# Kernel tuning notes

Measured on AMD Instinct MI355X. Metric: run time of the kernel, lower is better.

Reference implementation:

```python
import jax, jax.numpy as jnp
import numpy as np

# Architecture constants (match init_kwargs)
A = 4            # num_areas
E_PER = 512      # excitatory units per area
I_PER = 128      # inhibitory units per area
H = A * (E_PER + I_PER)   # 2560 hidden units, order: [all E (area-major), all I]
NUM_OBJS = 2
IN_UNITS = 64
IN = NUM_OBJS * IN_UNITS  # 128 input units
DT, TAU_X = 0.02, 0.1
ALPHA_X = DT / TAU_X


def _build_masks():
    """Signed Dale's-law connectivity masks, as in _get_connectivity_mask_* ."""
    # inter-area recurrent connectivity: nearest-neighbor hierarchy + self
    rec = np.eye(A) + np.eye(A, k=1) + np.eye(A, k=-1)
    ee = np.kron(rec, np.ones((E_PER, E_PER)))
    ei = np.kron(np.eye(A), np.ones((E_PER, I_PER)))   # E<-I only within area
    ie = np.kron(rec, np.ones((I_PER, E_PER)))
    ii = np.kron(np.eye(A), np.ones((I_PER, I_PER)))
    conn = np.block([[ee, ei], [ie, ii]])
    # sign mask: first e_size columns excitatory (+1), rest inhibitory (-1)
    sign = np.concatenate([np.ones(A * E_PER), -np.ones(A * I_PER)])[None, :]
    rec_mask = conn * sign
    np.fill_diagonal(rec_mask, 0.0)  # remove_diag=True in h2h EILinear
    # input mask: only area 0 receives external input; e_prop=1 for x2h (all +1)
    in_area = np.zeros((A, NUM_OBJS)); in_area[0, :] = 1.0
    in_e = np.kron(in_area, np.ones((E_PER, IN_UNITS)))
    in_i = np.kron(in_area, np.ones((I_PER, IN_UNITS)))
    in_mask = np.concatenate([in_e, in_i], axis=0)
    return jnp.asarray(rec_mask, jnp.float32), jnp.asarray(in_mask, jnp.float32)


def setup_inputs() -> dict:
    key = jax.random.key(0)
    k1, k2, k3 = jax.random.split(key, 3)
    T, B = 500, 64
    inputs = jax.random.normal(k1, (T, B, IN), dtype=jnp.float32)
    W_rec = jax.random.normal(k2, (H, H), dtype=jnp.float32) / np.sqrt(H)
    b_rec = jnp.zeros((H,), dtype=jnp.float32)
    W_in = jax.random.normal(k3, (H, IN), dtype=jnp.float32) / np.sqrt(IN)
    return {"inputs": inputs, "W_rec": W_rec, "b_rec": b_rec, "W_in": W_in}


def reference(inputs, W_rec, b_rec, W_in):
    rec_mask, in_mask = _build_masks()
    # EILinear effective weights: pos_func=abs, times signed connectivity mask
    W_rec_eff = jnp.abs(W_rec) * rec_mask          # [H, H]
    W_in_eff = jnp.abs(W_in) * in_mask             # [H, IN]
    # input projection for all timesteps at once
    proj = jnp.einsum('tbi,hi->tbh', inputs, W_in_eff)  # [T, B, H]

    def retanh(x):
        return jnp.tanh(jax.nn.relu(x))

    def step(carry, u_t):
        x, r = carry
        pre = r @ W_rec_eff.T + b_rec + u_t        # h2h(r) + x2h(u)
        x = (1.0 - ALPHA_X) * x + ALPHA_X * pre    # leaky integration
        r = retanh(x)
        return (x, r), r

    B = inputs.shape[1]
    x0 = jnp.zeros((B, H), dtype=inputs.dtype)     # x0 (train_init_state=False)
    (_, _), rates = jax.lax.scan(step, (x0, retanh(x0)), proj)
    return rates  # [T, B, H] firing rates
```

## Files before the change

kernel.cpp:

```cpp
#include <hip/hip_runtime.h>
#include <math.h>

#define Hn   2560
#define Bn   64
#define INW  128
#define ETOT 2048
#define HGn  160
#define MAXC 13
#define NBLK 160
#define MAXI 7
#define RFSTRIDE (80 * 4 * 512)

typedef __attribute__((ext_vector_type(8))) _Float16 half8;
typedef __attribute__((ext_vector_type(4))) float  floatx4;

__global__ void build_apack(const float* __restrict__ Wrec,
                            const float* __restrict__ Win,
                            _Float16* __restrict__ Af) {
  int hg = blockIdx.x, c = blockIdx.y;
  int a = (hg < 128) ? (hg >> 5) : ((hg - 128) >> 3);
  int nE = (a == 0 || a == 3) ? 8 : 12;
  int nch = nE + 1 + (a == 0 ? 1 : 0);
  if (c >= nch) return;
  int h0 = hg * 16;
  int tid = threadIdx.x;
  int kq = tid >> 6, L = tid & 63;
  int m = L & 15, q = L >> 4;
  int h = h0 + m;

  const float* src; int k0, stride; float sgn; bool isIn = false;
  if (c < nE)       { k0 = ((a == 0 ? 0 : a - 1) << 9) + (c << 7); src = Wrec; stride = Hn;  sgn =  1.f; }
  else if (c == nE) { k0 = ETOT + (a << 7);                        src = Wrec; stride = Hn;  sgn = -1.f; }
  else              { k0 = 0;                                      src = Win;  stride = INW; sgn =  1.f; isIn = true; }

  _Float16 hi8[8], lo8[8];
  #pragma unroll
  for (int j = 0; j < 8; ++j) {
    int k = k0 + kq * 32 + q * 8 + j;
    float w = fabsf(src[(size_t)h * stride + k]);
    if (!isIn && k == h) w = 0.f;
    w *= sgn;
    _Float16 wh = (_Float16)w;
    hi8[j] = wh;
    lo8[j] = (_Float16)(w - (float)wh);
  }
  _Float16* outp = Af + (size_t)(hg * MAXC + c) * 4096;
  *(uint4*)(outp + (kq * 2 + 0) * 512 + L * 8) = *(const uint4*)hi8;
  *(uint4*)(outp + (kq * 2 + 1) * 512 + L * 8) = *(const uint4*)lo8;
}

#define LOAD4(B0,B1,B2,B3,P) \
  asm volatile("global_load_dwordx4 %0, %4, off sc0 sc1\n\t" \
               "global_load_dwordx4 %1, %4, off offset:1024 sc0 sc1\n\t" \
               "global_load_dwordx4 %2, %4, off offset:2048 sc0 sc1\n\t" \
               "global_load_dwordx4 %3, %4, off offset:3072 sc0 sc1\n\t" \
               "s_waitcnt vmcnt(0)" \
               : "=&v"(B0), "=&v"(B1), "=&v"(B2), "=&v"(B3) \
               : "v"(P) : "memory")

#define LOAD8(X0,X1,X2,X3,Y0,Y1,Y2,Y3,PA,PB) \
  asm volatile("global_load_dwordx4 %0, %8, off sc0 sc1\n\t" \
               "global_load_dwordx4 %1, %8, off offset:1024 sc0 sc1\n\t" \
               "global_load_dwordx4 %2, %8, off offset:2048 sc0 sc1\n\t" \
               "global_load_dwordx4 %3, %8, off offset:3072 sc0 sc1\n\t" \
               "global_load_dwordx4 %4, %9, off sc0 sc1\n\t" \
               "global_load_dwordx4 %5, %9, off offset:1024 sc0 sc1\n\t" \
               "global_load_dwordx4 %6, %9, off offset:2048 sc0 sc1\n\t" \
               "global_load_dwordx4 %7, %9, off offset:3072 sc0 sc1\n\t" \
               "s_waitcnt vmcnt(0)" \
               : "=&v"(X0), "=&v"(X1), "=&v"(X2), "=&v"(X3), \
                 "=&v"(Y0), "=&v"(Y1), "=&v"(Y2), "=&v"(Y3) \
               : "v"(PA), "v"(PB) : "memory")

#define MFMA8(i, B0,B1,B2,B3) do { \
  ac0 = __builtin_amdgcn_mfma_f32_16x16x32_f16(ah[i], B0, ac0, 0, 0, 0); \
  ac0 = __builtin_amdgcn_mfma_f32_16x16x32_f16(al[i], B0, ac0, 0, 0, 0); \
  ac1 = __builtin_amdgcn_mfma_f32_16x16x32_f16(ah[i], B1, ac1, 0, 0, 0); \
  ac1 = __builtin_amdgcn_mfma_f32_16x16x32_f16(al[i], B1, ac1, 0, 0, 0); \
  ac2 = __builtin_amdgcn_mfma_f32_16x16x32_f16(ah[i], B2, ac2, 0, 0, 0); \
  ac2 = __builtin_amdgcn_mfma_f32_16x16x32_f16(al[i], B2, ac2, 0, 0, 0); \
  ac3 = __builtin_amdgcn_mfma_f32_16x16x32_f16(ah[i], B3, ac3, 0, 0, 0); \
  ac3 = __builtin_amdgcn_mfma_f32_16x16x32_f16(al[i], B3, ac3, 0, 0, 0); \
} while (0)

#define RECPATH1(i) do { \
  half8 B0_, B1_, B2_, B3_; \
  const _Float16* pp_ = rs + boff[i]; \
  LOAD4(B0_, B1_, B2_, B3_, pp_); \
  MFMA8(i, B0_, B1_, B2_, B3_); \
} while (0)

#define INPATH(i) do { \
  const float* ip_ = inputs + (size_t)t * (Bn * INW) + boff[i]; \
  int nb_ = L & 15; \
  half8 B0_, B1_, B2_, B3_; \
  _Pragma("unroll") for (int j = 0; j < 8; ++j) B0_[j] = (_Float16)ip_[(nb_ +  0) * INW + j]; \
  _Pragma("unroll") for (int j = 0; j < 8; ++j) B1_[j] = (_Float16)ip_[(nb_ + 16) * INW + j]; \
  _Pragma("unroll") for (int j = 0; j < 8; ++j) B2_[j] = (_Float16)ip_[(nb_ + 32) * INW + j]; \
  _Pragma("unroll") for (int j = 0; j < 8; ++j) B3_[j] = (_Float16)ip_[(nb_ + 48) * INW + j]; \
  MFMA8(i, B0_, B1_, B2_, B3_); \
} while (0)

#define PAIR(i0, i1) do { \
  bool r0_ = act[i0] && !isin[i0]; \
  bool r1_ = act[i1] && !isin[i1]; \
  if (r0_ && r1_) { \
    half8 X0_,X1_,X2_,X3_,Y0_,Y1_,Y2_,Y3_; \
    const _Float16* pa_ = rs + boff[i0]; \
    const _Float16* pb_ = rs + boff[i1]; \
    LOAD8(X0_,X1_,X2_,X3_,Y0_,Y1_,Y2_,Y3_, pa_, pb_); \
    MFMA8(i0, X0_, X1_, X2_, X3_); \
    MFMA8(i1, Y0_, Y1_, Y2_, Y3_); \
  } else { \
    if (r0_) RECPATH1(i0); else if (act[i0]) INPATH(i0); \
    if (r1_) RECPATH1(i1); else if (act[i1]) INPATH(i1); \
  } \
} while (0)

template <int ROT>
__global__ __launch_bounds__(512, ROT ? 1 : 2) void rnn_persist(
    const _Float16* __restrict__ Af,
    const float* __restrict__ inputs,
    _Float16* __restrict__ rfbase,
    const float* __restrict__ brec,
    float* __restrict__ rates,
    unsigned* bar, int T)
{
  __shared__ float red[8][1056];
  __shared__ float rrt[16][68];
  __shared__ float bb[16];

  const int bid = blockIdx.x;
  int hg_;
  if (ROT) {
    int x = bid & 7, aa = x >> 1, idx = (x & 1) * 20 + (bid >> 3);
    hg_ = (idx < 32) ? (aa * 32 + idx) : (128 + aa * 8 + (idx - 32));
  } else {
    hg_ = bid;
  }
  const int hg  = hg_;
  const int tid = threadIdx.x;
  const int w   = tid >> 6, L = tid & 63;
  const int h0  = hg * 16;
  const int a   = (hg < 128) ? (hg >> 5) : ((hg - 128) >> 3);
  const int nE  = (a == 0 || a == 3) ? 8 : 12;
  const int SK  = (nE + 1 + (a == 0 ? 1 : 0)) * 4;
  const int ktE0 = (a == 0 ? 0 : a - 1) * 16;
  const int ktI0 = 64 + a * 4;

  unsigned* bsub = bar + (hg & 7) * 64;
  unsigned* bmas = bar + 8 * 64;
  unsigned* bgen = bar + (9 + (hg & 7)) * 64;

  if (tid < 16) bb[tid] = brec[h0 + tid];

  half8 ah[MAXI], al[MAXI];
  int   boff[MAXI];
  bool  act[MAXI], isin[MAXI];
  const _Float16* Abase = Af + (size_t)hg * MAXC * 4096;
  #pragma unroll
  for (int i = 0; i < MAXI; ++i) {
    half8 zz = {0,0,0,0,0,0,0,0};
    ah[i] = zz; al[i] = zz;
    int ks = w + i * 8;
    act[i]  = ks < SK;
    isin[i] = false;
    boff[i] = 0;
    if (act[i]) {
      int c = ks >> 2, kq = ks & 3;
      const _Float16* Ap = Abase + (size_t)c * 4096 + (size_t)(kq * 2) * 512 + (size_t)L * 8;
      ah[i] = *(const half8*)Ap;
      al[i] = *(const half8*)(Ap + 512);
      if (c <= nE) {
        int kt = (c < nE) ? (ktE0 + c * 4 + kq) : (ktI0 + kq);
        boff[i] = kt * 2048 + L * 8;
      } else {
        isin[i] = true;
        boff[i] = kq * 32 + (L >> 4) * 8;
      }
    }
  }
  #pragma unroll
  for (int i = 0; i < MAXI; ++i)
    asm volatile("" : "+v"(ah[i]), "+v"(al[i]));

  float xv[2] = {0.f, 0.f};

  __syncthreads();

  for (int t = 0; t < T; ++t) {
    const _Float16* __restrict__ rs;
    _Float16* __restrict__ rd;
    if (ROT) {
      rs = rfbase + (size_t)t * RFSTRIDE;
      rd = rfbase + (size_t)(t + 1) * RFSTRIDE;
    } else {
      rs = (t & 1) ? (rfbase + RFSTRIDE) : rfbase;
      rd = (t & 1) ? rfbase : (rfbase + RFSTRIDE);
    }

    floatx4 ac0 = {0.f,0.f,0.f,0.f}, ac1 = {0.f,0.f,0.f,0.f};
    floatx4 ac2 = {0.f,0.f,0.f,0.f}, ac3 = {0.f,0.f,0.f,0.f};

    if (ROT) {
      #pragma unroll
      for (int i = 0; i < MAXI; ++i) {
        if (!act[i]) continue;
        half8 b0, b1, b2, b3;
        if (isin[i]) {
          const float* ip = inputs + (size_t)t * (Bn * INW) + boff[i];
          int nb = L & 15;
          #pragma unroll
          for (int j = 0; j < 8; ++j) b0[j] = (_Float16)ip[(nb +  0) * INW + j];
          #pragma unroll
          for (int j = 0; j < 8; ++j) b1[j] = (_Float16)ip[(nb + 16) * INW + j];
          #pragma unroll
          for (int j = 0; j < 8; ++j) b2[j] = (_Float16)ip[(nb + 32) * INW + j];
          #pragma unroll
          for (int j = 0; j < 8; ++j) b3[j] = (_Float16)ip[(nb + 48) * INW + j];
        } else {
          const _Float16* Bp = rs + boff[i];
          b0 = *(const half8*)(Bp);
          b1 = *(const half8*)(Bp + 512);
          b2 = *(const half8*)(Bp + 1024);
          b3 = *(const half8*)(Bp + 1536);
        }
        MFMA8(i, b0, b1, b2, b3);
      }
    } else {
      PAIR(0, 1);
      PAIR(2, 3);
      PAIR(4, 5);
      if (act[6]) { if (!isin[6]) RECPATH1(6); else INPATH(6); }
    }

    #pragma unroll
    for (int p = 0; p < 4; ++p) {
      int m = (L >> 4) * 4 + p;
      float* rw = &red[w][m * 66 + (L & 15)];
      rw[ 0] = ac0[p];
      rw[16] = ac1[p];
      rw[32] = ac2[p];
      rw[48] = ac3[p];
    }
    __syncthreads();

    #pragma unroll
    for (int e = 0; e < 2; ++e) {
      int elem = tid + e * 512;
      int m = elem >> 6, n = elem & 63;
      float s = 0.f;
      #pragma unroll
      for (int j = 0; j < 8; ++j) s += red[j][m * 66 + n];
      float x = 0.8f * xv[e] + 0.2f * (s + bb[m]);
      xv[e] = x;
      float xr = fmaxf(x, 0.f);
      float e2 = __builtin_amdgcn_exp2f(xr * 2.885390081777926814f);
      rrt[m][n] = 1.0f - 2.0f * __builtin_amdgcn_rcpf(e2 + 1.0f);
    }
    __syncthreads();

    if (tid < 128) {
      int bt = tid >> 5, Lq = tid & 31;
      int Lp = (hg & 1) * 32 + Lq;
      half8 vv;
      #pragma unroll
      for (int j = 0; j < 8; ++j)
        vv[j] = (_Float16)rrt[(Lq >> 4) * 8 + j][bt * 16 + (Lq & 15)];
      _Float16* dst = rd + (size_t)((hg >> 1) * 4 + bt) * 512 + (size_t)Lp * 8;
      asm volatile("global_store_dwordx4 %0, %1, off sc0 sc1\n\t"
                   "s_waitcnt vmcnt(0)"
                   :: "v"(dst), "v"(vv) : "memory");
    }
    __syncthreads();

    unsigned g = (unsigned)(t + 1);
    if (t + 1 < T && tid == 0) {
      unsigned s = __hip_atomic_fetch_add(bsub, 1u, __ATOMIC_RELAXED,
                                          __HIP_MEMORY_SCOPE_AGENT);
      if (s == g * 20u - 1u) {
        unsigned m2 = __hip_atomic_fetch_add(bmas, 1u, __ATOMIC_RELAXED,
                                             __HIP_MEMORY_SCOPE_AGENT);
        if (m2 == g * 8u - 1u) {
          #pragma unroll
          for (int x = 0; x < 8; ++x)
            __hip_atomic_store(bar + (9 + x) * 64, g, __ATOMIC_RELAXED,
                               __HIP_MEMORY_SCOPE_AGENT);
        }
      }
    }

    if (tid >= 256) {
      int tt = tid - 256;
      int b = tt >> 2, hq = tt & 3;
      floatx4 o;
      o.x = rrt[hq * 4 + 0][b];
      o.y = rrt[hq * 4 + 1][b];
      o.z = rrt[hq * 4 + 2][b];
      o.w = rrt[hq * 4 + 3][b];
      __builtin_nontemporal_store(o,
          (floatx4*)(rates + (size_t)t * (Bn * Hn) + (size_t)b * Hn + h0 + hq * 4));
    }

    if (t + 1 < T) {
      if (tid == 0) {
        while (__hip_atomic_load(bgen, __ATOMIC_RELAXED,
                                 __HIP_MEMORY_SCOPE_AGENT) < g)
          __builtin_amdgcn_s_sleep(2);
      }
      __syncthreads();
    }
  }
}

extern "C" void kernel_launch(void* const* d_in, const int* in_sizes, int n_in,
                              void* d_out, int out_size, void* d_ws, size_t ws_size,
                              hipStream_t stream) {
  const float* inputs = (const float*)d_in[0];
  const float* Wrec   = (const float*)d_in[1];
  const float* brec   = (const float*)d_in[2];
  const float* Win    = (const float*)d_in[3];
  int T = in_sizes[0] / (Bn * INW);

  const size_t afBytes  = (size_t)HGn * MAXC * 4096 * 2;
  const size_t slotB    = (size_t)RFSTRIDE * 2;
  const size_t rotBytes = (size_t)(T + 1) * slotB;
  const size_t barBytes = 8192;

  char* base = (char*)d_ws;
  _Float16* Af = (_Float16*)base;
  _Float16* rf = (_Float16*)(base + afBytes);

  const bool rot = ws_size >= afBytes + rotBytes + barBytes + (1u << 20);
  const size_t rfBytes = rot ? rotBytes : 2 * slotB;
  unsigned* bar = (unsigned*)(base + afBytes + rfBytes);

  (void)hipMemsetAsync(rf, 0, slotB, stream);
  (void)hipMemsetAsync(bar, 0, barBytes, stream);

  build_apack<<<dim3(HGn, MAXC), 256, 0, stream>>>(Wrec, Win, Af);

  float* rates = (float*)d_out;
  if (rot)
    rnn_persist<1><<<NBLK, 512, 0, stream>>>(Af, inputs, rf, brec, rates, bar, T);
  else
    rnn_persist<0><<<NBLK, 512, 0, stream>>>(Af, inputs, rf, brec, rates, bar, T);
}
```

Measured before the change: 2.701 ms.

## Replace hierarchical grid barrier with flat per-wave counters polled by one wave

Removes the two-level barrier (per-subgroup counter, then master counter, then generation broadcast). Each storing wave now atomically increments its subgroup counter right after its store, with no extra __syncthreads, and wave 0 polls all 8 subgroup counters in parallel with one lane per counter until each reaches (t+1)*40. This takes the serial atomic chain and the broadcast out of the critical path of every timestep. In exchange it adds more polling traffic on 8 counters.

```diff
diff --git a/kernel.cpp b/kernel.cpp
--- a/kernel.cpp
+++ b/kernel.cpp
@@ -6,8 +6,8 @@
 #define INW  128
 #define ETOT 2048
 #define HGn  160
+#define NBLK 160
 #define MAXC 13
-#define NBLK 160
 #define MAXI 7
 #define RFSTRIDE (80 * 4 * 512)
 
@@ -149,8 +149,6 @@
   const int ktI0 = 64 + a * 4;
 
   unsigned* bsub = bar + (hg & 7) * 64;
-  unsigned* bmas = bar + 8 * 64;
-  unsigned* bgen = bar + (9 + (hg & 7)) * 64;
 
   if (tid < 16) bb[tid] = brec[h0 + tid];
 
@@ -271,23 +269,9 @@
       asm volatile("global_store_dwordx4 %0, %1, off sc0 sc1\n\t"
                    "s_waitcnt vmcnt(0)"
                    :: "v"(dst), "v"(vv) : "memory");
-    }
-    __syncthreads();
-
-    unsigned g = (unsigned)(t + 1);
-    if (t + 1 < T && tid == 0) {
-      unsigned s = __hip_atomic_fetch_add(bsub, 1u, __ATOMIC_RELAXED,
-                                          __HIP_MEMORY_SCOPE_AGENT);
-      if (s == g * 20u - 1u) {
-        unsigned m2 = __hip_atomic_fetch_add(bmas, 1u, __ATOMIC_RELAXED,
-                                             __HIP_MEMORY_SCOPE_AGENT);
-        if (m2 == g * 8u - 1u) {
-          #pragma unroll
-          for (int x = 0; x < 8; ++x)
-            __hip_atomic_store(bar + (9 + x) * 64, g, __ATOMIC_RELAXED,
+      if ((t + 1 < T) && ((tid & 63) == 0))
+        __hip_atomic_fetch_add(bsub, 1u, __ATOMIC_RELAXED,
                                __HIP_MEMORY_SCOPE_AGENT);
-        }
-      }
     }
 
     if (tid >= 256) {
@@ -303,10 +287,15 @@
     }
 
     if (t + 1 < T) {
-      if (tid == 0) {
-        while (__hip_atomic_load(bgen, __ATOMIC_RELAXED,
-                                 __HIP_MEMORY_SCOPE_AGENT) < g)
-          __builtin_amdgcn_s_sleep(2);
+      if (w == 0) {
+        unsigned tgt = (unsigned)(t + 1) * 40u;
+        bool mine = (L >= 8);
+        while (!__all(mine)) {
+          if (!mine)
+            mine = (__hip_atomic_load(bar + L * 64, __ATOMIC_RELAXED,
+                                      __HIP_MEMORY_SCOPE_AGENT) >= tgt);
+          if (!__all(mine)) __builtin_amdgcn_s_sleep(1);
+        }
       }
       __syncthreads();
     }
```

New measurement: 3.608 ms. 33.6% more time.
